# Kernel tuning notes

Measured on AMD Instinct MI355X. Metric: run time of the kernel, lower is better.

Reference implementation:

```python
import jax, jax.numpy as jnp
import numpy as np

D_MODEL = 512
N_HEADS = 8
D_HEAD = D_MODEL // N_HEADS
EPS = 1e-6


def setup_inputs() -> dict:
    key = jax.random.key(0)
    ks = jax.random.split(key, 9)
    B, S = 2, 2048
    scale = 0.02
    x = jax.random.normal(ks[0], (B, S, D_MODEL), dtype=jnp.float32)
    Wq = jax.random.normal(ks[1], (D_MODEL, D_MODEL), dtype=jnp.float32) * scale
    Wk = jax.random.normal(ks[2], (D_MODEL, D_MODEL), dtype=jnp.float32) * scale
    Wv = jax.random.normal(ks[3], (D_MODEL, D_MODEL), dtype=jnp.float32) * scale
    Wo = jax.random.normal(ks[4], (D_MODEL, D_MODEL), dtype=jnp.float32) * scale
    bq = jax.random.normal(ks[5], (D_MODEL,), dtype=jnp.float32) * scale
    bk = jax.random.normal(ks[6], (D_MODEL,), dtype=jnp.float32) * scale
    bv = jax.random.normal(ks[7], (D_MODEL,), dtype=jnp.float32) * scale
    bo = jax.random.normal(ks[8], (D_MODEL,), dtype=jnp.float32) * scale
    return {"x": x, "Wq": Wq, "bq": bq, "Wk": Wk, "bk": bk,
            "Wv": Wv, "bv": bv, "Wo": Wo, "bo": bo}


def _split_heads(t, B, S):
    # [B,S,D] -> [B,H,S,dh]
    return t.reshape(B, S, N_HEADS, D_HEAD).transpose(0, 2, 1, 3)


def reference(x, Wq, bq, Wk, bk, Wv, bv, Wo, bo):
    B, S, _ = x.shape
    q = _split_heads(x @ Wq.T + bq, B, S)
    k = _split_heads(x @ Wk.T + bk, B, S)
    v = _split_heads(x @ Wv.T + bv, B, S)
    # 'relu' kernel applied to Q and K
    q = jax.nn.relu(q)
    k = jax.nn.relu(k)
    # K_sum: [B,H,S,1] -- per-position sum over head dim; note it broadcasts
    # over the KEY axis of attn, i.e. each QUERY row n is divided by K_sum[n]
    k_sum = k.sum(axis=-1, keepdims=True)
    attn = jnp.einsum('bhnd,bhmd->bhnm', q, k) / (k_sum + EPS)
    attn = jax.nn.softmax(attn, axis=-1)
    out = jnp.einsum('bhnm,bhmd->bhnd', attn, v)
    out = out.transpose(0, 2, 1, 3).reshape(B, S, D_MODEL)
    return (out @ Wo.T + bo, attn)
```

## Files before the change

### kernel.cpp

```cpp
#include <hip/hip_runtime.h>
#include <stdint.h>


typedef __attribute__((ext_vector_type(8))) short short8;
typedef __attribute__((ext_vector_type(4))) float f4;

#define MFMA(a, b, c) __builtin_amdgcn_mfma_f32_16x16x32_bf16(a, b, c, 0, 0, 0)

struct __align__(8) us4 { uint16_t a, b, c, d; };

__device__ __forceinline__ uint16_t f2bf(float f) {
  union { float f; uint32_t u; } v; v.f = f;
  uint32_t u = v.u;
  return (uint16_t)((u + 0x7fffu + ((u >> 16) & 1u)) >> 16);
}
__device__ __forceinline__ float bf2f(uint16_t u) {
  union { uint32_t u; float f; } v; v.u = ((uint32_t)u) << 16; return v.f;
}
__device__ __forceinline__ us4 pack4(float4 v) {
  us4 r; r.a = f2bf(v.x); r.b = f2bf(v.y); r.c = f2bf(v.z); r.d = f2bf(v.w); return r;
}

__device__ __forceinline__ void async16(const uint16_t* g, uint16_t* l) {
  __builtin_amdgcn_global_load_lds(
      (const __attribute__((address_space(1))) void*)g,
      (__attribute__((address_space(3))) void*)l, 16, 0, 0);
}

__global__ __launch_bounds__(256) void convert_kernel(
    const float* __restrict__ x, const float* __restrict__ Wq,
    const float* __restrict__ Wk, const float* __restrict__ Wv,
    const float* __restrict__ Wo, uint16_t* __restrict__ xb,
    uint16_t* __restrict__ W3, uint16_t* __restrict__ Wob) {
  int i = blockIdx.x * 256 + threadIdx.x;
  ((us4*)xb)[i] = pack4(((const float4*)x)[i]);
  if (i < 65536) {
    ((us4*)W3)[i]          = pack4(((const float4*)Wq)[i]);
    ((us4*)W3)[65536 + i]  = pack4(((const float4*)Wk)[i]);
    ((us4*)W3)[131072 + i] = pack4(((const float4*)Wv)[i]);
    ((us4*)Wob)[i]         = pack4(((const float4*)Wo)[i]);
  }
}

__device__ __forceinline__ void gemm_loop(
    const uint16_t* __restrict__ A, const uint16_t* __restrict__ Bt,
    int row0, int col0, uint16_t* A0, uint16_t* B0,
    uint16_t* A1, uint16_t* B1, f4 (&acc)[4][4]) {
  const int tid = threadIdx.x;
  const int w = tid >> 6, lane = tid & 63;
  const int c = lane & 15, quad = lane >> 4;
  const int wm = w >> 1, wn = w & 1;
  const int srow = lane >> 2;
  const int sslot = ((lane & 3) ^ ((lane >> 2) & 3) ^ ((lane >> 4) & 3)) * 8;
  const uint16_t* Asrc = A + (size_t)(row0 + srow) * 512 + sslot;
  const uint16_t* Bsrc = Bt + (size_t)(col0 + srow) * 512 + sslot;
  const int posv = (quad ^ (c & 3) ^ (c >> 2)) * 8;
#pragma unroll
  for (int chh = 0; chh < 2; ++chh) {
    int ch = w * 2 + chh;
    async16(Asrc + (size_t)ch * 16 * 512, A0 + ch * 512);
    async16(Bsrc + (size_t)ch * 16 * 512, B0 + ch * 512);
  }
  __syncthreads();
  for (int k0 = 0; k0 < 512; k0 += 32) {
    const uint16_t* Ac = (k0 & 32) ? A1 : A0;
    const uint16_t* Bc = (k0 & 32) ? B1 : B0;
    if (k0 + 32 < 512) {
      uint16_t* An = (k0 & 32) ? A0 : A1;
      uint16_t* Bn = (k0 & 32) ? B0 : B1;
#pragma unroll
      for (int chh = 0; chh < 2; ++chh) {
        int ch = w * 2 + chh;
        async16(Asrc + (size_t)ch * 16 * 512 + (k0 + 32), An + ch * 512);
        async16(Bsrc + (size_t)ch * 16 * 512 + (k0 + 32), Bn + ch * 512);
      }
    }
    short8 af[4], bfr[4];
#pragma unroll
    for (int mi = 0; mi < 4; ++mi)
      af[mi] = *(const short8*)&Ac[(wm * 64 + mi * 16 + c) * 32 + posv];
#pragma unroll
    for (int ni = 0; ni < 4; ++ni)
      bfr[ni] = *(const short8*)&Bc[(wn * 64 + ni * 16 + c) * 32 + posv];
#pragma unroll
    for (int mi = 0; mi < 4; ++mi)
#pragma unroll
      for (int ni = 0; ni < 4; ++ni)
        acc[mi][ni] = MFMA(af[mi], bfr[ni], acc[mi][ni]);
    __syncthreads();
  }
}

__global__ __launch_bounds__(256) void qkv_gemm(
    const uint16_t* __restrict__ xb, const uint16_t* __restrict__ W3,
    const float* __restrict__ bq, const float* __restrict__ bk,
    const float* __restrict__ bv, uint16_t* __restrict__ Qb,
    uint16_t* __restrict__ Kb, uint16_t* __restrict__ Vt) {
  __shared__ __align__(16) uint16_t smem[25600];
  uint16_t* A0 = smem;
  uint16_t* B0 = smem + 4096;
  uint16_t* A1 = smem + 8192;
  uint16_t* B1 = smem + 12288;
  uint16_t* Ct = smem + 8192;
  f4 acc[4][4] = {};
  const int row0 = blockIdx.y * 128, col0 = blockIdx.x * 128;
  gemm_loop(xb, W3, row0, col0, A0, B0, A1, B1, acc);
  const int tid = threadIdx.x, w = tid >> 6, lane = tid & 63;
  const int c = lane & 15, quad = lane >> 4;
  const int wm = w >> 1, wn = w & 1;
  const int r3 = col0 >> 9;
  if (r3 < 2) {
    const float* bias = (r3 == 0) ? bq : bk;
    uint16_t* dst = (r3 == 0) ? Qb : Kb;
#pragma unroll
    for (int mi = 0; mi < 4; ++mi)
#pragma unroll
      for (int ni = 0; ni < 4; ++ni)
#pragma unroll
        for (int r = 0; r < 4; ++r) {
          int row = row0 + wm * 64 + mi * 16 + quad * 4 + r;
          int col = col0 + wn * 64 + ni * 16 + c;
          int o = col & 511;
          float v = acc[mi][ni][r] + bias[o];
          dst[(size_t)row * 512 + o] = f2bf(fmaxf(v, 0.0f));
        }
  } else {
#pragma unroll
    for (int mi = 0; mi < 4; ++mi)
#pragma unroll
      for (int ni = 0; ni < 4; ++ni)
#pragma unroll
        for (int r = 0; r < 4; ++r) {
          int sl = wm * 64 + mi * 16 + quad * 4 + r;
          int cl = wn * 64 + ni * 16 + c;
          int o = (col0 + cl) & 511;
          Ct[sl * 136 + cl] = f2bf(acc[mi][ni][r] + bv[o]);
        }
    __syncthreads();
    const int b = row0 >> 11, s0 = row0 & 2047;
    const int cl = tid >> 1, half = tid & 1;
    const int ocol = (col0 - 1024) + cl;
    uint16_t* vdst = Vt + (size_t)(b * 512 + ocol) * 2048 + s0 + half * 64;
#pragma unroll
    for (int g = 0; g < 8; ++g) {
      union { short8 v; uint16_t e[8]; } o8;
#pragma unroll
      for (int jj = 0; jj < 8; ++jj)
        o8.e[jj] = Ct[(half * 64 + g * 8 + jj) * 136 + cl];
      *(short8*)(vdst + g * 8) = o8.v;
    }
  }
}

__global__ __launch_bounds__(256) void proj_gemm(
    const uint16_t* __restrict__ Ob, const uint16_t* __restrict__ Wob,
    const float* __restrict__ bo, float* __restrict__ out) {
  __shared__ __align__(16) uint16_t smem[16384];
  uint16_t* A0 = smem;
  uint16_t* B0 = smem + 4096;
  uint16_t* A1 = smem + 8192;
  uint16_t* B1 = smem + 12288;
  f4 acc[4][4] = {};
  const int row0 = blockIdx.y * 128, col0 = blockIdx.x * 128;
  gemm_loop(Ob, Wob, row0, col0, A0, B0, A1, B1, acc);
  const int tid = threadIdx.x, w = tid >> 6, lane = tid & 63;
  const int c = lane & 15, quad = lane >> 4;
  const int wm = w >> 1, wn = w & 1;
#pragma unroll
  for (int mi = 0; mi < 4; ++mi)
#pragma unroll
    for (int ni = 0; ni < 4; ++ni)
#pragma unroll
      for (int r = 0; r < 4; ++r) {
        int row = row0 + wm * 64 + mi * 16 + quad * 4 + r;
        int col = col0 + wn * 64 + ni * 16 + c;
        out[(size_t)row * 512 + col] = acc[mi][ni][r] + bo[col];
      }
}

__global__ __launch_bounds__(256) void ksum_kernel(
    const uint16_t* __restrict__ Kb, float* __restrict__ rq) {
  int t = blockIdx.x * 256 + threadIdx.x;
  int row = t >> 2, part = t & 3;
  const uint4* p = (const uint4*)(Kb + (size_t)row * 64 + part * 16);
  float s = 0.f;
#pragma unroll
  for (int g = 0; g < 2; ++g) {
    union { uint4 u; uint16_t e[8]; } v; v.u = p[g];
#pragma unroll
    for (int j = 0; j < 8; ++j) s += bf2f(v.e[j]);
  }
  s += __shfl_xor(s, 1, 4);
  s += __shfl_xor(s, 2, 4);
  if (part == 0) rq[row] = 1.0f / (s + 1e-6f);
}

__global__ __launch_bounds__(256) void attn_kernel(
    const uint16_t* __restrict__ Qb, const uint16_t* __restrict__ Kb,
    const uint16_t* __restrict__ Vt, const float* __restrict__ rq,
    float* __restrict__ attn, uint16_t* __restrict__ Ob) {
  __shared__ __align__(16) uint16_t Klds[2][64 * 64];
  __shared__ __align__(16) uint16_t Vlds[2][64 * 64];
  __shared__ __align__(16) float Pw[4][16 * 64];
  const int tid = threadIdx.x, w = tid >> 6, lane = tid & 63;
  const int c = lane & 15, quad = lane >> 4, c7 = c & 7;
  const int bid = blockIdx.x;
  const int bh = (bid & 7) * 2 + ((bid >> 3) & 1);
  const int qt = bid >> 4;
  const int b = bh >> 3, h = bh & 7;
  const int n0 = qt * 64;
  const int rbase = b * 2048 + n0;
  const uint16_t* qptr = Qb + (size_t)(rbase + w * 16 + c) * 512 + h * 64 + quad * 8;
  short8 aq0 = *(const short8*)qptr;
  short8 aq1 = *(const short8*)(qptr + 32);
  float rqv[4];
#pragma unroll
  for (int r = 0; r < 4; ++r)
    rqv[r] = rq[(size_t)(rbase + w * 16 + quad * 4 + r) * 8 + h];
  const int vsrow = lane >> 3;
  const int vslot = ((lane & 7) ^ vsrow) * 8;
  const uint16_t* Ksrc = Kb + (size_t)(b * 2048) * 512 + h * 64 + vslot;
  const uint16_t* Vsrc = Vt + (size_t)(bh * 64) * 2048 + vslot;

  float lsum[4] = {0.f, 0.f, 0.f, 0.f};
#pragma unroll
  for (int chh = 0; chh < 2; ++chh) {
    int ch = w * 2 + chh;
    async16(Ksrc + (size_t)(ch * 8 + vsrow) * 512, Klds[0] + ch * 512);
  }
  __syncthreads();
  for (int kt = 0; kt < 32; ++kt) {
    const uint16_t* Kc = Klds[kt & 1];
    if (kt < 31) {
      uint16_t* Kn = Klds[(kt & 1) ^ 1];
#pragma unroll
      for (int chh = 0; chh < 2; ++chh) {
        int ch = w * 2 + chh;
        async16(Ksrc + (size_t)((kt + 1) * 64 + ch * 8 + vsrow) * 512,
                Kn + ch * 512);
      }
    }
#pragma unroll
    for (int ni = 0; ni < 4; ++ni) {
      const uint16_t* kp = &Kc[(ni * 16 + c) * 64];
      short8 bk0 = *(const short8*)(kp + ((quad ^ c7) * 8));
      short8 bk1 = *(const short8*)(kp + (((quad + 4) ^ c7) * 8));
      f4 s = {};
      s = MFMA(aq0, bk0, s);
      s = MFMA(aq1, bk1, s);
#pragma unroll
      for (int r = 0; r < 4; ++r) lsum[r] += __expf(s[r] * rqv[r]);
    }
    __syncthreads();
  }
  float rli[4];
#pragma unroll
  for (int r = 0; r < 4; ++r) {
    float v = lsum[r];
    v += __shfl_xor(v, 1, 16);
    v += __shfl_xor(v, 2, 16);
    v += __shfl_xor(v, 4, 16);
    v += __shfl_xor(v, 8, 16);
    rli[r] = 1.0f / v;
  }

  f4 oacc[4] = {};
  float* arowc = attn + ((size_t)bh * 2048 + n0 + w * 16 + c) * 2048;
  float* Pme = Pw[w];
#pragma unroll
  for (int chh = 0; chh < 2; ++chh) {
    int ch = w * 2 + chh;
    async16(Ksrc + (size_t)(ch * 8 + vsrow) * 512, Klds[0] + ch * 512);
    async16(Vsrc + (size_t)(ch * 8 + vsrow) * 2048, Vlds[0] + ch * 512);
  }
  __syncthreads();
  for (int kt = 0; kt < 32; ++kt) {
    const int cur = kt & 1;
    const uint16_t* Kc = Klds[cur];
    const uint16_t* Vc = Vlds[cur];
    if (kt < 31) {
      uint16_t* Kn = Klds[cur ^ 1];
      uint16_t* Vn = Vlds[cur ^ 1];
#pragma unroll
      for (int chh = 0; chh < 2; ++chh) {
        int ch = w * 2 + chh;
        async16(Ksrc + (size_t)((kt + 1) * 64 + ch * 8 + vsrow) * 512,
                Kn + ch * 512);
        async16(Vsrc + (size_t)(ch * 8 + vsrow) * 2048 + (kt + 1) * 64,
                Vn + ch * 512);
      }
    }
#pragma unroll
    for (int ni = 0; ni < 4; ++ni) {
      const uint16_t* kp = &Kc[(ni * 16 + c) * 64];
      short8 bk0 = *(const short8*)(kp + ((quad ^ c7) * 8));
      short8 bk1 = *(const short8*)(kp + (((quad + 4) ^ c7) * 8));
      f4 s = {};
      s = MFMA(aq0, bk0, s);
      s = MFMA(aq1, bk1, s);
#pragma unroll
      for (int r = 0; r < 4; ++r) {
        int rowp = quad * 4 + r;
        float p = __expf(s[r] * rqv[r]) * rli[r];
        Pme[rowp * 64 + (((ni * 4 + (c >> 2)) ^ rowp) * 4) + (c & 3)] = p;
      }
    }
    asm volatile("s_waitcnt lgkmcnt(0)" ::: "memory");
#pragma unroll
    for (int ks = 0; ks < 2; ++ks) {
      int ch0 = ks * 8 + quad * 2;
      f4 p0 = *(const f4*)&Pme[c * 64 + ((ch0 ^ c) * 4)];
      f4 p1 = *(const f4*)&Pme[c * 64 + (((ch0 + 1) ^ c) * 4)];
      *(f4*)&arowc[kt * 64 + ch0 * 4] = p0;
      *(f4*)&arowc[kt * 64 + ch0 * 4 + 4] = p1;
      union { short8 v; uint16_t e[8]; } ap;
#pragma unroll
      for (int i = 0; i < 4; ++i) { ap.e[i] = f2bf(p0[i]); ap.e[4 + i] = f2bf(p1[i]); }
#pragma unroll
      for (int nj = 0; nj < 4; ++nj) {
        short8 bvv = *(const short8*)&Vc[(nj * 16 + c) * 64 +
                                         (((ks * 4 + quad) ^ c7) * 8)];
        oacc[nj] = MFMA(ap.v, bvv, oacc[nj]);
      }
    }
    __syncthreads();
  }
#pragma unroll
  for (int nj = 0; nj < 4; ++nj)
#pragma unroll
    for (int r = 0; r < 4; ++r)
      Ob[(size_t)(rbase + w * 16 + quad * 4 + r) * 512 + h * 64 + nj * 16 + c] =
          f2bf(oacc[nj][r]);
}

extern "C" void kernel_launch(void* const* d_in, const int* in_sizes, int n_in,
                              void* d_out, int out_size, void* d_ws, size_t ws_size,
                              hipStream_t stream) {
  const float* x  = (const float*)d_in[0];
  const float* Wq = (const float*)d_in[1];
  const float* bq = (const float*)d_in[2];
  const float* Wk = (const float*)d_in[3];
  const float* bk = (const float*)d_in[4];
  const float* Wv = (const float*)d_in[5];
  const float* bv = (const float*)d_in[6];
  const float* Wo = (const float*)d_in[7];
  const float* bo = (const float*)d_in[8];

  float* out0 = (float*)d_out;
  float* attn = out0 + (size_t)2 * 2048 * 512;

  uint8_t* ws = (uint8_t*)d_ws;
  uint16_t* xb  = (uint16_t*)(ws);
  uint16_t* W3  = (uint16_t*)(ws + 0x400000);
  uint16_t* Wob = (uint16_t*)(ws + 0x580000);
  uint16_t* Qb  = (uint16_t*)(ws + 0x600000);
  uint16_t* Kb  = (uint16_t*)(ws + 0xA00000);
  uint16_t* Vt  = (uint16_t*)(ws + 0xE00000);
  uint16_t* Ob  = (uint16_t*)(ws + 0x1200000);
  float*    rq  = (float*)  (ws + 0x1600000);

  convert_kernel<<<2048, 256, 0, stream>>>(x, Wq, Wk, Wv, Wo, xb, W3, Wob);
  qkv_gemm<<<dim3(12, 32), 256, 0, stream>>>(xb, W3, bq, bk, bv, Qb, Kb, Vt);
  ksum_kernel<<<512, 256, 0, stream>>>(Kb, rq);
  attn_kernel<<<512, 256, 0, stream>>>(Qb, Kb, Vt, rq, attn, Ob);
  proj_gemm<<<dim3(4, 32), 256, 0, stream>>>(Ob, Wob, bo, out0);
}
```

Baseline: 378.6 us.

## Fuse K row-sum into QKV epilogue and transpose score MFMA for direct attn stores

The per-head K sum and its reciprocal are now computed in the QKV GEMM epilogue with a 16-lane shuffle reduction, which removes the separate ksum kernel and its re-read of K. In the attention kernel the score MFMA operands are swapped so each lane holds four consecutive key columns of one query row. The fp32 attention probabilities can then be written straight to global with nontemporal vector stores, and only a bf16 copy goes through LDS for the PV MFMA, which halves the LDS staging size. The row softmax sum now reduces across quads with two shuffles, and the global write pattern changes from 8-float chunks to 4-float chunks per lane.

```diff
diff --git a/kernel.cpp b/kernel.cpp
--- a/kernel.cpp
+++ b/kernel.cpp
@@ -95,7 +95,8 @@
     const uint16_t* __restrict__ xb, const uint16_t* __restrict__ W3,
     const float* __restrict__ bq, const float* __restrict__ bk,
     const float* __restrict__ bv, uint16_t* __restrict__ Qb,
-    uint16_t* __restrict__ Kb, uint16_t* __restrict__ Vt) {
+    uint16_t* __restrict__ Kb, uint16_t* __restrict__ Vt,
+    float* __restrict__ rq) {
   __shared__ __align__(16) uint16_t smem[25600];
   uint16_t* A0 = smem;
   uint16_t* B0 = smem + 4096;
@@ -109,9 +110,7 @@
   const int c = lane & 15, quad = lane >> 4;
   const int wm = w >> 1, wn = w & 1;
   const int r3 = col0 >> 9;
-  if (r3 < 2) {
-    const float* bias = (r3 == 0) ? bq : bk;
-    uint16_t* dst = (r3 == 0) ? Qb : Kb;
+  if (r3 == 0) {
 #pragma unroll
     for (int mi = 0; mi < 4; ++mi)
 #pragma unroll
@@ -121,9 +120,31 @@
           int row = row0 + wm * 64 + mi * 16 + quad * 4 + r;
           int col = col0 + wn * 64 + ni * 16 + c;
           int o = col & 511;
-          float v = acc[mi][ni][r] + bias[o];
-          dst[(size_t)row * 512 + o] = f2bf(fmaxf(v, 0.0f));
+          float v = acc[mi][ni][r] + bq[o];
+          Qb[(size_t)row * 512 + o] = f2bf(fmaxf(v, 0.0f));
         }
+  } else if (r3 == 1) {
+    const int hh = ((col0 & 511) >> 6) + wn;
+#pragma unroll
+    for (int mi = 0; mi < 4; ++mi)
+#pragma unroll
+      for (int r = 0; r < 4; ++r) {
+        int row = row0 + wm * 64 + mi * 16 + quad * 4 + r;
+        float s = 0.f;
+#pragma unroll
+        for (int ni = 0; ni < 4; ++ni) {
+          int col = col0 + wn * 64 + ni * 16 + c;
+          int o = col & 511;
+          float v = fmaxf(acc[mi][ni][r] + bk[o], 0.0f);
+          Kb[(size_t)row * 512 + o] = f2bf(v);
+          s += v;
+        }
+        s += __shfl_xor(s, 1, 16);
+        s += __shfl_xor(s, 2, 16);
+        s += __shfl_xor(s, 4, 16);
+        s += __shfl_xor(s, 8, 16);
+        if (c == 0) rq[(size_t)row * 8 + hh] = 1.0f / (s + 1e-6f);
+      }
   } else {
 #pragma unroll
     for (int mi = 0; mi < 4; ++mi)
@@ -178,30 +199,13 @@
       }
 }
 
-__global__ __launch_bounds__(256) void ksum_kernel(
-    const uint16_t* __restrict__ Kb, float* __restrict__ rq) {
-  int t = blockIdx.x * 256 + threadIdx.x;
-  int row = t >> 2, part = t & 3;
-  const uint4* p = (const uint4*)(Kb + (size_t)row * 64 + part * 16);
-  float s = 0.f;
-#pragma unroll
-  for (int g = 0; g < 2; ++g) {
-    union { uint4 u; uint16_t e[8]; } v; v.u = p[g];
-#pragma unroll
-    for (int j = 0; j < 8; ++j) s += bf2f(v.e[j]);
-  }
-  s += __shfl_xor(s, 1, 4);
-  s += __shfl_xor(s, 2, 4);
-  if (part == 0) rq[row] = 1.0f / (s + 1e-6f);
-}
-
 __global__ __launch_bounds__(256) void attn_kernel(
     const uint16_t* __restrict__ Qb, const uint16_t* __restrict__ Kb,
     const uint16_t* __restrict__ Vt, const float* __restrict__ rq,
     float* __restrict__ attn, uint16_t* __restrict__ Ob) {
   __shared__ __align__(16) uint16_t Klds[2][64 * 64];
   __shared__ __align__(16) uint16_t Vlds[2][64 * 64];
-  __shared__ __align__(16) float Pw[4][16 * 64];
+  __shared__ __align__(16) uint16_t Pw[4][16 * 64];
   const int tid = threadIdx.x, w = tid >> 6, lane = tid & 63;
   const int c = lane & 15, quad = lane >> 4, c7 = c & 7;
   const int bid = blockIdx.x;
@@ -213,16 +217,13 @@
   const uint16_t* qptr = Qb + (size_t)(rbase + w * 16 + c) * 512 + h * 64 + quad * 8;
   short8 aq0 = *(const short8*)qptr;
   short8 aq1 = *(const short8*)(qptr + 32);
-  float rqv[4];
-#pragma unroll
-  for (int r = 0; r < 4; ++r)
-    rqv[r] = rq[(size_t)(rbase + w * 16 + quad * 4 + r) * 8 + h];
+  const float rqv = rq[(size_t)(rbase + w * 16 + c) * 8 + h];
   const int vsrow = lane >> 3;
   const int vslot = ((lane & 7) ^ vsrow) * 8;
   const uint16_t* Ksrc = Kb + (size_t)(b * 2048) * 512 + h * 64 + vslot;
   const uint16_t* Vsrc = Vt + (size_t)(bh * 64) * 2048 + vslot;
 
-  float lsum[4] = {0.f, 0.f, 0.f, 0.f};
+  float lsum = 0.f;
 #pragma unroll
   for (int chh = 0; chh < 2; ++chh) {
     int ch = w * 2 + chh;
@@ -246,27 +247,20 @@
       short8 bk0 = *(const short8*)(kp + ((quad ^ c7) * 8));
       short8 bk1 = *(const short8*)(kp + (((quad + 4) ^ c7) * 8));
       f4 s = {};
-      s = MFMA(aq0, bk0, s);
-      s = MFMA(aq1, bk1, s);
-#pragma unroll
-      for (int r = 0; r < 4; ++r) lsum[r] += __expf(s[r] * rqv[r]);
+      s = MFMA(bk0, aq0, s);
+      s = MFMA(bk1, aq1, s);
+#pragma unroll
+      for (int r = 0; r < 4; ++r) lsum += __expf(s[r] * rqv);
     }
     __syncthreads();
   }
-  float rli[4];
-#pragma unroll
-  for (int r = 0; r < 4; ++r) {
-    float v = lsum[r];
-    v += __shfl_xor(v, 1, 16);
-    v += __shfl_xor(v, 2, 16);
-    v += __shfl_xor(v, 4, 16);
-    v += __shfl_xor(v, 8, 16);
-    rli[r] = 1.0f / v;
-  }
+  lsum += __shfl_xor(lsum, 16);
+  lsum += __shfl_xor(lsum, 32);
+  const float rli = 1.0f / lsum;
 
   f4 oacc[4] = {};
-  float* arowc = attn + ((size_t)bh * 2048 + n0 + w * 16 + c) * 2048;
-  float* Pme = Pw[w];
+  float* arow = attn + ((size_t)bh * 2048 + n0 + w * 16 + c) * 2048;
+  uint16_t* Pme = Pw[w];
 #pragma unroll
   for (int chh = 0; chh < 2; ++chh) {
     int ch = w * 2 + chh;
@@ -296,31 +290,28 @@
       short8 bk0 = *(const short8*)(kp + ((quad ^ c7) * 8));
       short8 bk1 = *(const short8*)(kp + (((quad + 4) ^ c7) * 8));
       f4 s = {};
-      s = MFMA(aq0, bk0, s);
-      s = MFMA(aq1, bk1, s);
-#pragma unroll
-      for (int r = 0; r < 4; ++r) {
-        int rowp = quad * 4 + r;
-        float p = __expf(s[r] * rqv[r]) * rli[r];
-        Pme[rowp * 64 + (((ni * 4 + (c >> 2)) ^ rowp) * 4) + (c & 3)] = p;
-      }
+      s = MFMA(bk0, aq0, s);
+      s = MFMA(bk1, aq1, s);
+      f4 p;
+#pragma unroll
+      for (int r = 0; r < 4; ++r) p[r] = __expf(s[r] * rqv) * rli;
+      __builtin_nontemporal_store(p, (f4*)&arow[kt * 64 + ni * 16 + quad * 4]);
+      uint32_t q01 = (uint32_t)f2bf(p[0]) | ((uint32_t)f2bf(p[1]) << 16);
+      uint32_t q23 = (uint32_t)f2bf(p[2]) | ((uint32_t)f2bf(p[3]) << 16);
+      int slot_w = (ni * 2 + (quad >> 1)) ^ c7;
+      uint32_t* wp = (uint32_t*)&Pme[c * 64 + slot_w * 8 + (quad & 1) * 4];
+      wp[0] = q01;
+      wp[1] = q23;
     }
     asm volatile("s_waitcnt lgkmcnt(0)" ::: "memory");
 #pragma unroll
-    for (int ks = 0; ks < 2; ++ks) {
-      int ch0 = ks * 8 + quad * 2;
-      f4 p0 = *(const f4*)&Pme[c * 64 + ((ch0 ^ c) * 4)];
-      f4 p1 = *(const f4*)&Pme[c * 64 + (((ch0 + 1) ^ c) * 4)];
-      *(f4*)&arowc[kt * 64 + ch0 * 4] = p0;
-      *(f4*)&arowc[kt * 64 + ch0 * 4 + 4] = p1;
-      union { short8 v; uint16_t e[8]; } ap;
-#pragma unroll
-      for (int i = 0; i < 4; ++i) { ap.e[i] = f2bf(p0[i]); ap.e[4 + i] = f2bf(p1[i]); }
+    for (int m = 0; m < 2; ++m) {
+      short8 pa = *(const short8*)&Pme[c * 64 + (((m * 4 + quad) ^ c7) * 8)];
 #pragma unroll
       for (int nj = 0; nj < 4; ++nj) {
         short8 bvv = *(const short8*)&Vc[(nj * 16 + c) * 64 +
-                                         (((ks * 4 + quad) ^ c7) * 8)];
-        oacc[nj] = MFMA(ap.v, bvv, oacc[nj]);
+                                         (((m * 4 + quad) ^ c7) * 8)];
+        oacc[nj] = MFMA(pa, bvv, oacc[nj]);
       }
     }
     __syncthreads();
@@ -360,8 +351,7 @@
   float*    rq  = (float*)  (ws + 0x1600000);
 
   convert_kernel<<<2048, 256, 0, stream>>>(x, Wq, Wk, Wv, Wo, xb, W3, Wob);
-  qkv_gemm<<<dim3(12, 32), 256, 0, stream>>>(xb, W3, bq, bk, bv, Qb, Kb, Vt);
-  ksum_kernel<<<512, 256, 0, stream>>>(Kb, rq);
+  qkv_gemm<<<dim3(12, 32), 256, 0, stream>>>(xb, W3, bq, bk, bv, Qb, Kb, Vt, rq);
   attn_kernel<<<512, 256, 0, stream>>>(Qb, Kb, Vt, rq, attn, Ob);
   proj_gemm<<<dim3(4, 32), 256, 0, stream>>>(Ob, Wob, bo, out0);
 }
```

Result: slower. 391.6 us (+3.4%).
